# Performance work log

Hardware: AMD Instinct MI355X
Metric: run time of the kernel (lower is better)

## Reference

```python
import jax, jax.numpy as jnp
import numpy as np

N, D, H = 4096, 1024, 2048


def positional_encoding(d_model, n):
    even_i = jnp.arange(0, d_model, 2, dtype=jnp.float32)
    denom = jnp.power(jnp.float32(10000.0), even_i / d_model)
    pos = jnp.arange(n, dtype=jnp.float32)[:, None]            # (N,1)
    even_pe = jnp.sin(pos / denom)                             # (N,D/2)
    odd_pe = jnp.cos(pos / denom)                              # (N,D/2)
    # interleave sin/cos: stack on axis 2 then flatten -> (N, D)
    return jnp.stack([even_pe, odd_pe], axis=2).reshape(n, d_model)


def setup_inputs() -> dict:
    key = jax.random.key(0)
    ks = jax.random.split(key, 5)
    X = jax.random.normal(ks[0], (N, D), dtype=jnp.float32)
    mask = jnp.ones((N,), dtype=jnp.int32)  # unused by the module
    Wv = jax.random.normal(ks[1], (D, D), dtype=jnp.float32) * 0.02
    bv = jnp.zeros((D,), dtype=jnp.float32)
    W1 = jax.random.normal(ks[2], (2 * D, H), dtype=jnp.float32) * 0.02
    b1 = jnp.zeros((H,), dtype=jnp.float32)
    W2 = jax.random.normal(ks[3], (H, N), dtype=jnp.float32) * 0.02
    b2 = jnp.zeros((N,), dtype=jnp.float32)
    return {"X": X, "mask": mask, "Wv": Wv, "bv": bv,
            "W1": W1, "b1": b1, "W2": W2, "b2": b2}


def reference(X, mask, Wv, bv, W1, b1, W2, b2):
    n, d = X.shape
    V = X @ Wv + bv                                            # (N,D)
    PE = positional_encoding(d, n).astype(X.dtype)
    E = PE * X                                                 # (N,D)
    # leave-one-out mean: (global sum - row_i) / (N-1)  [replaces O(N^2) loop]
    loo = (jnp.sum(E, axis=0, keepdims=True) - E) / (n - 1)    # (N,D)
    feat = jnp.concatenate([X, loo], axis=1)                   # (N,2D)
    hidden = jax.nn.relu(feat @ W1 + b1)                       # (N,H)
    att_scores = hidden @ W2 + b2                              # (N,N)
    att_weights = jax.nn.softmax(att_scores, axis=-1)          # (N,N)
    # dropout p=0 (inference) -> identity
    return att_weights @ V                                     # (N,D)
```

## Files before the change

### kernel.cpp

```cpp
#include <hip/hip_runtime.h>
#include <hip/hip_bf16.h>

#define TOK 4096
#define DIM 1024
#define HID 2048
#define LN10K 9.210340371976184f

typedef __bf16 bh;
typedef __bf16 v8bf __attribute__((ext_vector_type(8)));
typedef float v4f __attribute__((ext_vector_type(4)));

typedef const __attribute__((address_space(1))) void* gvp;
typedef __attribute__((address_space(3))) void* svp;

__device__ __forceinline__ void gl_lds16(const bh* g, bh* s) {
  __builtin_amdgcn_global_load_lds((gvp)g, (svp)s, 16, 0, 0);
}


template <int BN, bool RELU, bool TROUT, bool EXPS, typename OutT>
__device__ __forceinline__ void gemm_bt_body(int id,
                                             const bh* __restrict__ A,
                                             const bh* __restrict__ BT,
                                             const float* __restrict__ bias,
                                             OutT* __restrict__ C,
                                             float* __restrict__ rowsum,
                                             int K, int lda, int ldbt, int ldc) {
  constexpr int NT = BN / 32;
  __shared__ bh As[128 * 64];
  __shared__ bh Bs[BN * 64];
  const int t = threadIdx.x;
  const int bm = (id & 31) * 128, bn = (id >> 5) * BN;

  const int srow = t >> 3;
  const int c8 = ((t & 7) ^ (srow & 7)) * 8;
  const bh* gA = A + (size_t)(bm + srow) * lda + c8;
  const bh* gB = BT + (size_t)(bn + srow) * ldbt + c8;
  bh* sA = As + t * 8;
  bh* sB = Bs + t * 8;

  const int lane = t & 63, w = t >> 6;
  const int wm = (w >> 1) * 64, wn = (w & 1) * (BN / 2);
  const int lc = lane & 15, q = lane >> 4;

  v4f acc[4][NT] = {};
  for (int k0 = 0; k0 < K; k0 += 64) {
#pragma unroll
    for (int j = 0; j < 4; ++j)
      gl_lds16(gA + k0 + j * 32 * lda, sA + j * 2048);
#pragma unroll
    for (int j = 0; j < BN / 32; ++j)
      gl_lds16(gB + k0 + j * 32 * ldbt, sB + j * 2048);
    __syncthreads();
#pragma unroll
    for (int h = 0; h < 2; ++h) {
      const int off = ((h * 4 + q) ^ (lc & 7)) * 8;
      v8bf af[4], bfr[NT];
#pragma unroll
      for (int mt = 0; mt < 4; ++mt)
        af[mt] = *(const v8bf*)(As + (wm + mt * 16 + lc) * 64 + off);
#pragma unroll
      for (int nt = 0; nt < NT; ++nt)
        bfr[nt] = *(const v8bf*)(Bs + (wn + nt * 16 + lc) * 64 + off);
#pragma unroll
      for (int mt = 0; mt < 4; ++mt)
#pragma unroll
        for (int nt = 0; nt < NT; ++nt)
          acc[mt][nt] = __builtin_amdgcn_mfma_f32_16x16x32_bf16(af[mt], bfr[nt], acc[mt][nt], 0, 0, 0);
    }
    __syncthreads();
  }

  const int r4 = q * 4;
  if (EXPS) {
    float bbv[NT];
#pragma unroll
    for (int nt = 0; nt < NT; ++nt)
      bbv[nt] = bias ? bias[bn + wn + nt * 16 + lc] : 0.0f;
#pragma unroll
    for (int mt = 0; mt < 4; ++mt) {
#pragma unroll
      for (int r = 0; r < 4; ++r) {
        int row = bm + wm + mt * 16 + r4 + r;
        float rs = 0.0f;
#pragma unroll
        for (int nt = 0; nt < NT; ++nt) {
          float val = __expf(acc[mt][nt][r] + bbv[nt]);
          rs += val;
          C[(size_t)row * ldc + bn + wn + nt * 16 + lc] = (OutT)val;
        }
        rs += __shfl_xor(rs, 1);
        rs += __shfl_xor(rs, 2);
        rs += __shfl_xor(rs, 4);
        rs += __shfl_xor(rs, 8);
        if (lc == 0) atomicAdd(rowsum + row, rs);
      }
    }
  } else if (TROUT) {
    bh* trs = As;
#pragma unroll
    for (int mt = 0; mt < 4; ++mt) {
#pragma unroll
      for (int nt = 0; nt < NT; ++nt) {
        int cl = wn + nt * 16 + lc;
        float bb = bias ? bias[bn + cl] : 0.0f;
#pragma unroll
        for (int r = 0; r < 4; ++r) {
          float val = acc[mt][nt][r] + bb;
          if (RELU) val = fmaxf(val, 0.0f);
          trs[cl * 128 + (wm + mt * 16 + r4 + r)] = (bh)val;
        }
      }
    }
    __syncthreads();
#pragma unroll
    for (int p = 0; p < 4; ++p) {
      int chunk = p * 256 + t;
      int vr = chunk >> 4, sc = chunk & 15;
      *(v8bf*)((bh*)C + (size_t)(bn + vr) * ldc + bm + sc * 8) =
          *(const v8bf*)(trs + vr * 128 + sc * 8);
    }
  } else {
#pragma unroll
    for (int mt = 0; mt < 4; ++mt) {
      int row0 = bm + wm + mt * 16 + r4;
#pragma unroll
      for (int nt = 0; nt < NT; ++nt) {
        int col = bn + wn + nt * 16 + lc;
        float bb = bias ? bias[col] : 0.0f;
#pragma unroll
        for (int r = 0; r < 4; ++r) {
          float val = acc[mt][nt][r] + bb;
          if (RELU) val = fmaxf(val, 0.0f);
          C[(size_t)(row0 + r) * ldc + col] = (OutT)val;
        }
      }
    }
  }
}

template <int BN, bool RELU, bool TROUT, bool EXPS, typename OutT>
__global__ __launch_bounds__(256, 2) void gemm_bt(const bh* __restrict__ A,
                                                  const bh* __restrict__ BT,
                                                  const float* __restrict__ bias,
                                                  OutT* __restrict__ C,
                                                  float* __restrict__ rowsum,
                                                  int K, int lda, int ldbt, int ldc) {
  gemm_bt_body<BN, RELU, TROUT, EXPS, OutT>(blockIdx.x, A, BT, bias, C, rowsum,
                                            K, lda, ldbt, ldc);
}

__global__ __launch_bounds__(256) void prep_and_transpose(
    const float* __restrict__ X, bh* __restrict__ featb, float* __restrict__ S,
    const float* __restrict__ Wv, const float* __restrict__ W1,
    const float* __restrict__ W2, bh* __restrict__ WvT, bh* __restrict__ W1T,
    bh* __restrict__ W2T) {
  __shared__ float tile[32][33];
  int bid = blockIdx.x;
  if (bid < 512) {
    int cp = (bid & 1) * 256 + threadIdx.x;
    int c = cp * 2;
    int r0 = (bid >> 1) * 16;
    float inv_denom = __expf(-(float)c * (LN10K / (float)DIM));
    float s0 = 0.f, s1 = 0.f;
#pragma unroll 4
    for (int r = r0; r < r0 + 16; ++r) {
      float2 x = *(const float2*)(X + (size_t)r * DIM + c);
      float sn, cs;
      __sincosf((float)r * inv_denom, &sn, &cs);
      s0 += sn * x.x;
      s1 += cs * x.y;
      bh pair[2] = {(bh)x.x, (bh)x.y};
      *(ushort2*)(featb + (size_t)r * (2 * DIM) + c) = *(ushort2*)pair;
    }
    atomicAdd(&S[c], s0);
    atomicAdd(&S[c + 1], s1);
    return;
  }
  bid -= 512;
  const float* in; bh* out; int Ncol, R, bx, by;
  if (bid < 1024)      { in = Wv; out = WvT; Ncol = DIM; R = DIM;
                         bx = bid & 31; by = bid >> 5; }
  else if (bid < 5120) { int b = bid - 1024; in = W1; out = W1T; Ncol = HID; R = 2 * DIM;
                         bx = b & 63; by = b >> 6; }
  else                 { int b = bid - 5120; in = W2; out = W2T; Ncol = TOK; R = HID;
                         bx = b & 127; by = b >> 7; }
  int nb = bx * 32, rb = by * 32;
  int tx = threadIdx.x & 31, ty = threadIdx.x >> 5;
#pragma unroll
  for (int j = 0; j < 32; j += 8)
    tile[ty + j][tx] = in[(size_t)(rb + ty + j) * Ncol + nb + tx];
  __syncthreads();
#pragma unroll
  for (int j = 0; j < 32; j += 8)
    out[(size_t)(nb + ty + j) * R + rb + tx] = (bh)tile[tx][ty + j];
}

__global__ __launch_bounds__(256, 2) void gemm1_and_loo(
    const bh* __restrict__ featb, const bh* __restrict__ WvT,
    const float* __restrict__ bv, bh* __restrict__ Vt,
    const float* __restrict__ X, const float* __restrict__ S,
    bh* __restrict__ featb_w) {
  int bid = blockIdx.x;
  if (bid < 512) {
    gemm_bt_body<64, false, true, false, bh>(bid, featb, WvT, bv, Vt, nullptr,
                                             DIM, 2 * DIM, DIM, TOK);
    return;
  }
  size_t e4 = ((size_t)(bid - 512) * 256 + threadIdx.x) * 4;
  int r = (int)(e4 >> 10);
  int c = (int)(e4 & 1023);
  float4 x = *(const float4*)(X + e4);
  float4 s = *(const float4*)(S + c);
  float id0 = __expf(-(float)c * (LN10K / (float)DIM));
  float id1 = __expf(-(float)(c + 2) * (LN10K / (float)DIM));
  float sn0, cs0, sn1, cs1;
  __sincosf((float)r * id0, &sn0, &cs0);
  __sincosf((float)r * id1, &sn1, &cs1);
  const float inv = 1.0f / (float)(TOK - 1);
  bh outv[4];
  outv[0] = (bh)((s.x - sn0 * x.x) * inv);
  outv[1] = (bh)((s.y - cs0 * x.y) * inv);
  outv[2] = (bh)((s.z - sn1 * x.z) * inv);
  outv[3] = (bh)((s.w - cs1 * x.w) * inv);
  *(ushort4*)(featb_w + (size_t)r * (2 * DIM) + DIM + c) = *(ushort4*)outv;
}

__global__ __launch_bounds__(256, 2) void gemm4_fused(const bh* __restrict__ A,
                                                      const bh* __restrict__ BT,
                                                      const float* __restrict__ rowsum,
                                                      float* __restrict__ out) {
  __shared__ bh As[64 * 64];
  __shared__ bh Bs[128 * 64];
  const int t = threadIdx.x;
  const int id = blockIdx.x;
  const int bm = (id & 63) * 64, bn = (id >> 6) * 128;

  const int sr = t >> 3;
  const int c8 = ((t & 7) ^ (sr & 7)) * 8;
  const bh* gA = A + (size_t)(bm + sr) * TOK + c8;
  const bh* gB = BT + (size_t)(bn + sr) * TOK + c8;
  bh* sA = As + t * 8;
  bh* sB = Bs + t * 8;

  const int lane = t & 63, w = t >> 6;
  const int wm = (w >> 1) * 32, wn = (w & 1) * 64;
  const int lc = lane & 15, q = lane >> 4;

  v4f acc[2][4] = {};
  for (int k0 = 0; k0 < TOK; k0 += 64) {
#pragma unroll
    for (int j = 0; j < 2; ++j)
      gl_lds16(gA + k0 + (size_t)(j * 32) * TOK, sA + j * 2048);
#pragma unroll
    for (int j = 0; j < 4; ++j)
      gl_lds16(gB + k0 + (size_t)(j * 32) * TOK, sB + j * 2048);
    __syncthreads();
#pragma unroll
    for (int h = 0; h < 2; ++h) {
      const int off = ((h * 4 + q) ^ (lc & 7)) * 8;
      v8bf af[2], bfr[4];
#pragma unroll
      for (int mt = 0; mt < 2; ++mt)
        af[mt] = *(const v8bf*)(As + (wm + mt * 16 + lc) * 64 + off);
#pragma unroll
      for (int nt = 0; nt < 4; ++nt)
        bfr[nt] = *(const v8bf*)(Bs + (wn + nt * 16 + lc) * 64 + off);
#pragma unroll
      for (int mt = 0; mt < 2; ++mt)
#pragma unroll
        for (int nt = 0; nt < 4; ++nt)
          acc[mt][nt] = __builtin_amdgcn_mfma_f32_16x16x32_bf16(af[mt], bfr[nt], acc[mt][nt], 0, 0, 0);
    }
    __syncthreads();
  }

  const int r4 = q * 4;
#pragma unroll
  for (int mt = 0; mt < 2; ++mt) {
#pragma unroll
    for (int r = 0; r < 4; ++r) {
      int row = bm + wm + mt * 16 + r4 + r;
      float inv = 1.0f / rowsum[row];
#pragma unroll
      for (int nt = 0; nt < 4; ++nt)
        out[(size_t)row * DIM + bn + wn + nt * 16 + lc] = acc[mt][nt][r] * inv;
    }
  }
}

extern "C" void kernel_launch(void* const* d_in, const int* in_sizes, int n_in,
                              void* d_out, int out_size, void* d_ws, size_t ws_size,
                              hipStream_t stream) {
  (void)in_sizes; (void)n_in; (void)out_size; (void)ws_size;
  const float* X  = (const float*)d_in[0];
  const float* Wv = (const float*)d_in[2];
  const float* bv = (const float*)d_in[3];
  const float* W1 = (const float*)d_in[4];
  const float* b1 = (const float*)d_in[5];
  const float* W2 = (const float*)d_in[6];
  const float* b2 = (const float*)d_in[7];
  float* out = (float*)d_out;

  char* ws = (char*)d_ws;
  bh* featb = (bh*)(ws);
  bh* WvT   = (bh*)(ws + (16u << 20));
  bh* W1T   = (bh*)(ws + (18u << 20));
  bh* W2T   = (bh*)(ws + (26u << 20));
  bh* Vt    = (bh*)(ws + (42u << 20));
  bh* hid   = (bh*)(ws + (50u << 20));
  bh* scr   = (bh*)(ws + (66u << 20));
  float* S  = (float*)(ws + (98u << 20));
  float* rowsum = (float*)(ws + (98u << 20) + 4096);

  hipError_t e = hipMemsetAsync(S, 0, 4096 + 4096 * sizeof(float), stream);
  (void)e;
  prep_and_transpose<<<dim3(512 + 1024 + 4096 + 8192), 256, 0, stream>>>(
      X, featb, S, Wv, W1, W2, WvT, W1T, W2T);
  gemm1_and_loo<<<dim3(512 + (TOK * DIM) / 1024), 256, 0, stream>>>(
      featb, WvT, bv, Vt, X, S, featb);
  gemm_bt<128, true, false, false, bh><<<dim3(32 * (HID / 128)), 256, 0, stream>>>(
      featb, W1T, b1, hid, nullptr, 2 * DIM, 2 * DIM, 2 * DIM, HID);
  gemm_bt<128, false, false, true, bh><<<dim3(32 * (TOK / 128)), 256, 0, stream>>>(
      hid, W2T, b2, scr, rowsum, HID, HID, HID, TOK);
  gemm4_fused<<<dim3(512), 256, 0, stream>>>(scr, Vt, rowsum, out);
}
```

Measured before the change: 303.4 us.

## Defer weight transposes into later GEMM launches to overlap with compute

The W1 and W2 fp32-to-bf16 transposes move out of the first prep kernel. Each now runs as extra blocks inside the launch just before the GEMM that needs it: W1 alongside GEMM1 and the leave-one-out step, W2 alongside GEMM2. This lets the memory-bound transpose work overlap with matrix-core GEMM blocks instead of running serially, and merges GEMM2 into a combined launch. The cost is heterogeneous blocks sharing one launch, with the 256-thread, 2-blocks-per-SM launch bounds applied to transpose blocks too, and possible load imbalance or tail effects.

After: 306.2 us. About the same (+0.9%).

```diff
diff --git a/kernel.cpp b/kernel.cpp
--- a/kernel.cpp
+++ b/kernel.cpp
@@ -17,6 +17,21 @@
   __builtin_amdgcn_global_load_lds((gvp)g, (svp)s, 16, 0, 0);
 }
 
+
+__device__ __forceinline__ void tr32(const float* __restrict__ in,
+                                     bh* __restrict__ out, int Ncol, int R,
+                                     int bx, int by) {
+  __shared__ float tile[32][33];
+  int nb = bx * 32, rb = by * 32;
+  int tx = threadIdx.x & 31, ty = threadIdx.x >> 5;
+#pragma unroll
+  for (int j = 0; j < 32; j += 8)
+    tile[ty + j][tx] = in[(size_t)(rb + ty + j) * Ncol + nb + tx];
+  __syncthreads();
+#pragma unroll
+  for (int j = 0; j < 32; j += 8)
+    out[(size_t)(nb + ty + j) * R + rb + tx] = (bh)tile[tx][ty + j];
+}
 
 template <int BN, bool RELU, bool TROUT, bool EXPS, typename OutT>
 __device__ __forceinline__ void gemm_bt_body(int id,
@@ -150,12 +165,9 @@
                                             K, lda, ldbt, ldc);
 }
 
-__global__ __launch_bounds__(256) void prep_and_transpose(
+__global__ __launch_bounds__(256) void prep_trWv(
     const float* __restrict__ X, bh* __restrict__ featb, float* __restrict__ S,
-    const float* __restrict__ Wv, const float* __restrict__ W1,
-    const float* __restrict__ W2, bh* __restrict__ WvT, bh* __restrict__ W1T,
-    bh* __restrict__ W2T) {
-  __shared__ float tile[32][33];
+    const float* __restrict__ Wv, bh* __restrict__ WvT) {
   int bid = blockIdx.x;
   if (bid < 512) {
     int cp = (bid & 1) * 256 + threadIdx.x;
@@ -177,53 +189,58 @@
     atomicAdd(&S[c + 1], s1);
     return;
   }
-  bid -= 512;
-  const float* in; bh* out; int Ncol, R, bx, by;
-  if (bid < 1024)      { in = Wv; out = WvT; Ncol = DIM; R = DIM;
-                         bx = bid & 31; by = bid >> 5; }
-  else if (bid < 5120) { int b = bid - 1024; in = W1; out = W1T; Ncol = HID; R = 2 * DIM;
-                         bx = b & 63; by = b >> 6; }
-  else                 { int b = bid - 5120; in = W2; out = W2T; Ncol = TOK; R = HID;
-                         bx = b & 127; by = b >> 7; }
-  int nb = bx * 32, rb = by * 32;
-  int tx = threadIdx.x & 31, ty = threadIdx.x >> 5;
-#pragma unroll
-  for (int j = 0; j < 32; j += 8)
-    tile[ty + j][tx] = in[(size_t)(rb + ty + j) * Ncol + nb + tx];
-  __syncthreads();
-#pragma unroll
-  for (int j = 0; j < 32; j += 8)
-    out[(size_t)(nb + ty + j) * R + rb + tx] = (bh)tile[tx][ty + j];
-}
-
-__global__ __launch_bounds__(256, 2) void gemm1_and_loo(
+  int b = bid - 512;
+  tr32(Wv, WvT, DIM, DIM, b & 31, b >> 5);
+}
+
+__global__ __launch_bounds__(256, 2) void gemm1_loo_trW1(
     const bh* __restrict__ featb, const bh* __restrict__ WvT,
     const float* __restrict__ bv, bh* __restrict__ Vt,
     const float* __restrict__ X, const float* __restrict__ S,
-    bh* __restrict__ featb_w) {
+    bh* __restrict__ featb_w, const float* __restrict__ W1,
+    bh* __restrict__ W1T) {
   int bid = blockIdx.x;
   if (bid < 512) {
     gemm_bt_body<64, false, true, false, bh>(bid, featb, WvT, bv, Vt, nullptr,
                                              DIM, 2 * DIM, DIM, TOK);
     return;
   }
-  size_t e4 = ((size_t)(bid - 512) * 256 + threadIdx.x) * 4;
-  int r = (int)(e4 >> 10);
-  int c = (int)(e4 & 1023);
-  float4 x = *(const float4*)(X + e4);
-  float4 s = *(const float4*)(S + c);
-  float id0 = __expf(-(float)c * (LN10K / (float)DIM));
-  float id1 = __expf(-(float)(c + 2) * (LN10K / (float)DIM));
-  float sn0, cs0, sn1, cs1;
-  __sincosf((float)r * id0, &sn0, &cs0);
-  __sincosf((float)r * id1, &sn1, &cs1);
-  const float inv = 1.0f / (float)(TOK - 1);
-  bh outv[4];
-  outv[0] = (bh)((s.x - sn0 * x.x) * inv);
-  outv[1] = (bh)((s.y - cs0 * x.y) * inv);
-  outv[2] = (bh)((s.z - sn1 * x.z) * inv);
-  outv[3] = (bh)((s.w - cs1 * x.w) * inv);
-  *(ushort4*)(featb_w + (size_t)r * (2 * DIM) + DIM + c) = *(ushort4*)outv;
+  if (bid < 4608) {
+    size_t e4 = ((size_t)(bid - 512) * 256 + threadIdx.x) * 4;
+    int r = (int)(e4 >> 10);
+    int c = (int)(e4 & 1023);
+    float4 x = *(const float4*)(X + e4);
+    float4 s = *(const float4*)(S + c);
+    float id0 = __expf(-(float)c * (LN10K / (float)DIM));
+    float id1 = __expf(-(float)(c + 2) * (LN10K / (float)DIM));
+    float sn0, cs0, sn1, cs1;
+    __sincosf((float)r * id0, &sn0, &cs0);
+    __sincosf((float)r * id1, &sn1, &cs1);
+    const float inv = 1.0f / (float)(TOK - 1);
+    bh outv[4];
+    outv[0] = (bh)((s.x - sn0 * x.x) * inv);
+    outv[1] = (bh)((s.y - cs0 * x.y) * inv);
+    outv[2] = (bh)((s.z - sn1 * x.z) * inv);
+    outv[3] = (bh)((s.w - cs1 * x.w) * inv);
+    *(ushort4*)(featb_w + (size_t)r * (2 * DIM) + DIM + c) = *(ushort4*)outv;
+    return;
+  }
+  int b = bid - 4608;
+  tr32(W1, W1T, HID, 2 * DIM, b & 63, b >> 6);
+}
+
+__global__ __launch_bounds__(256, 2) void gemm2_trW2(
+    const bh* __restrict__ featb, const bh* __restrict__ W1T,
+    const float* __restrict__ b1, bh* __restrict__ hid,
+    const float* __restrict__ W2, bh* __restrict__ W2T) {
+  int bid = blockIdx.x;
+  if (bid < 512) {
+    gemm_bt_body<128, true, false, false, bh>(bid, featb, W1T, b1, hid, nullptr,
+                                              2 * DIM, 2 * DIM, 2 * DIM, HID);
+    return;
+  }
+  int b = bid - 512;
+  tr32(W2, W2T, TOK, HID, b & 127, b >> 7);
 }
 
 __global__ __launch_bounds__(256, 2) void gemm4_fused(const bh* __restrict__ A,
@@ -315,12 +332,10 @@
 
   hipError_t e = hipMemsetAsync(S, 0, 4096 + 4096 * sizeof(float), stream);
   (void)e;
-  prep_and_transpose<<<dim3(512 + 1024 + 4096 + 8192), 256, 0, stream>>>(
-      X, featb, S, Wv, W1, W2, WvT, W1T, W2T);
-  gemm1_and_loo<<<dim3(512 + (TOK * DIM) / 1024), 256, 0, stream>>>(
-      featb, WvT, bv, Vt, X, S, featb);
-  gemm_bt<128, true, false, false, bh><<<dim3(32 * (HID / 128)), 256, 0, stream>>>(
-      featb, W1T, b1, hid, nullptr, 2 * DIM, 2 * DIM, 2 * DIM, HID);
+  prep_trWv<<<dim3(512 + 1024), 256, 0, stream>>>(X, featb, S, Wv, WvT);
+  gemm1_loo_trW1<<<dim3(512 + 4096 + 4096), 256, 0, stream>>>(
+      featb, WvT, bv, Vt, X, S, featb, W1, W1T);
+  gemm2_trW2<<<dim3(512 + 8192), 256, 0, stream>>>(featb, W1T, b1, hid, W2, W2T);
   gemm_bt<128, false, false, true, bh><<<dim3(32 * (TOK / 128)), 256, 0, stream>>>(
       hid, W2T, b2, scr, rowsum, HID, HID, HID, TOK);
   gemm4_fused<<<dim3(512), 256, 0, stream>>>(scr, Vt, rowsum, out);
```
